# Performance work log

Measured on AMD Instinct MI355X. Metric: run time of the kernel, lower is better.

Reference implementation:

```python
import jax, jax.numpy as jnp
import numpy as np

N, D, E = 16384, 2048, 64   # tokens, d_model, num_experts
K = 9                        # self.k = min(k+1, num_experts) with k=8
EPS = 0.01
SIGMA = 1.0 / E              # Normal(0, 1/num_experts) stddev


def setup_inputs() -> dict:
    key = jax.random.key(0)
    ks = jax.random.split(key, 6)
    x = jax.random.normal(ks[0], (N, D), jnp.float32)
    Wr = jax.random.normal(ks[1], (D, E), jnp.float32) * 0.02
    br = jnp.zeros((E,), jnp.float32)
    Wn = jax.random.normal(ks[2], (D, E), jnp.float32) * 0.02
    bn = jnp.zeros((E,), jnp.float32)
    noise_eps = jax.random.normal(ks[3], (N, E), jnp.float32)
    # torch: (-empty.exponential_()).log() -> log of Exp(1) samples
    gumbel_noise = jnp.log(jax.random.exponential(ks[4], (N, E), jnp.float32))
    return {"x": x, "Wr": Wr, "br": br, "Wn": Wn, "bn": bn,
            "noise_eps": noise_eps, "gumbel_noise": gumbel_noise}


def reference(x, Wr, br, Wn, bn, noise_eps, gumbel_noise):
    raw_logits = x @ Wr + br                              # [N, E]
    noise_stddev = jax.nn.softplus(x @ Wn + bn) + EPS     # [N, E]
    noisy_logits = raw_logits + noise_eps * noise_stddev  # [N, E]

    top_vals, top_idx = jax.lax.top_k(noisy_logits, K)    # [N, K] sorted desc
    # scatter ones at top-k indices (indices unique per row)
    hard_mask = jax.nn.one_hot(top_idx, E, dtype=noisy_logits.dtype).sum(axis=1)  # [N, E]

    # gumbel-softmax straight-through relaxation
    mask_soft = jax.nn.softmax(noisy_logits + gumbel_noise, axis=-1)
    expert_mask = hard_mask - jax.lax.stop_gradient(mask_soft) + mask_soft

    route_prob = jax.nn.softmax(noisy_logits, axis=-1)    # [N, E]
    importance = jax.nn.softmax(raw_logits, axis=-1).sum(axis=0)  # [E]

    # load: P(raw + noise > threshold), Normal(0, 1/E) CDF per original
    threshold = top_vals[:, K - 1]                        # [N]
    z = (threshold[:, None] - raw_logits) / noise_stddev  # [N, E]
    cdf = 0.5 * (1.0 + jax.scipy.special.erf(z / (SIGMA * jnp.sqrt(jnp.float32(2.0)))))
    load = (1.0 - cdf).sum(axis=0)                        # [E]

    return (expert_mask, route_prob, importance, load)
```

## Files before the change

kernel.cpp:

```cpp
#include <hip/hip_runtime.h>
#include <hip/hip_bf16.h>
#include <math.h>

#define N_TOK 16384
#define DIM   2048
#define NE    64
#define TOPK  9

#define ROWS     32
#define DC       64
#define NCHUNK   (DIM / DC)
#define NTHREADS 256

typedef short  short8  __attribute__((ext_vector_type(8)));
typedef float  float4_ __attribute__((ext_vector_type(4)));
typedef unsigned short ushort_t;

__device__ __forceinline__ void async16(const void* g, void* l) {
    __builtin_amdgcn_global_load_lds(
        (const __attribute__((address_space(1))) void*)g,
        (__attribute__((address_space(3))) void*)l, 16, 0, 0);
}

__device__ __forceinline__ unsigned pk2(float a, float b) {
    float2 f; f.x = a; f.y = b;
    __hip_bfloat162 h = __float22bfloat162_rn(f);
    unsigned u;
    __builtin_memcpy(&u, &h, 4);
    return u;
}

__device__ __forceinline__ void cvt8(const float4_ va, const float4_ vb,
                                     short8* h, short8* l) {
    union { short8 s; unsigned u[4]; } H, L;
    const float f[8] = {va[0], va[1], va[2], va[3], vb[0], vb[1], vb[2], vb[3]};
#pragma unroll
    for (int i = 0; i < 4; ++i) {
        const float a = f[2 * i], b = f[2 * i + 1];
        const unsigned p = pk2(a, b);
        H.u[i] = p;
        const float ha = __uint_as_float(p << 16);
        const float hb = __uint_as_float(p & 0xffff0000u);
        L.u[i] = pk2(a - ha, b - hb);
    }
    *h = H.s; *l = L.s;
}

__device__ __forceinline__ float wave_max64(float v) {
#pragma unroll
    for (int off = 32; off > 0; off >>= 1)
        v = fmaxf(v, __shfl_xor(v, off, 64));
    return v;
}
__device__ __forceinline__ float wave_sum64(float v) {
#pragma unroll
    for (int off = 32; off > 0; off >>= 1)
        v += __shfl_xor(v, off, 64);
    return v;
}

__global__ __launch_bounds__(256)
void prep_w(const float* __restrict__ Wr, const float* __restrict__ Wn,
            ushort_t* __restrict__ wsW)
{
    const int gid = blockIdx.x * 256 + threadIdx.x;
    const int l   = gid & 63;
    const int ct  = (gid >> 6) & 7;
    const int kcg = gid >> 9;
    const int n   = ct * 16 + (l & 15);
    const int k0  = kcg * 32 + (l >> 4) * 8;
    const float* src = (n < NE) ? (Wr + n) : (Wn + (n - NE));
    union { short8 s; ushort_t us[8]; } H, L;
#pragma unroll
    for (int j = 0; j < 8; ++j) {
        const float v = src[(size_t)(k0 + j) * NE];
        const unsigned uv = __float_as_uint(v);
        const unsigned hb = (uv + 0x7fffu + ((uv >> 16) & 1u)) & 0xffff0000u;
        const float lo = v - __uint_as_float(hb);
        const unsigned ul = __float_as_uint(lo);
        H.us[j] = (ushort_t)(hb >> 16);
        L.us[j] = (ushort_t)((ul + 0x7fffu + ((ul >> 16) & 1u)) >> 16);
    }
    const size_t s0 = (size_t)(kcg * 8 + ct) * 2;
    *(short8*)(wsW + s0 * 512 + l * 8)         = H.s;
    *(short8*)(wsW + (s0 + 1) * 512 + l * 8)   = L.s;
}

__global__ __launch_bounds__(NTHREADS, 3)
void moe_main(const float* __restrict__ x,
              const float* __restrict__ br,
              const float* __restrict__ bn,
              const float* __restrict__ noise_eps,
              const float* __restrict__ gumbel,
              const ushort_t* __restrict__ wsW,
              float* __restrict__ out)
{
    __shared__ __align__(16) float smem[4352];

    const int t    = threadIdx.x;
    const int lane = t & 63;
    const int w    = t >> 6;
    const int c4   = lane & 15;
    const int q    = lane >> 4;
    const int row0 = blockIdx.x * ROWS;

    const float* gxp[2];
    int lxo[2];
#pragma unroll
    for (int ii = 0; ii < 2; ++ii) {
        const int i  = 2 * w + ii;
        const int r  = 4 * i + q;
        const int gk = c4 ^ (r & 15);
        gxp[ii] = x + (size_t)(row0 + r) * DIM + gk * 4;
        lxo[ii] = i * 256;
    }

    int aoff[2][2];
#pragma unroll
    for (int kc = 0; kc < 2; ++kc) {
        const int g0 = kc * 8 + q * 2;
        aoff[kc][0] = c4 * 64 + ((g0 ^ c4) * 4);
        aoff[kc][1] = c4 * 64 + (((g0 + 1) ^ c4) * 4);
    }

    float4_ acc[2][2];
#pragma unroll
    for (int rt = 0; rt < 2; ++rt)
#pragma unroll
        for (int cc = 0; cc < 2; ++cc)
            acc[rt][cc] = (float4_)(0.f);

    const char* wsB = (const char*)wsW;

#pragma unroll
    for (int ii = 0; ii < 2; ++ii) { async16(gxp[ii], &smem[lxo[ii]]); gxp[ii] += DC; }

    for (int ch = 0; ch < NCHUNK; ++ch) {
        __syncthreads();
        const int b = ch & 1;
        short8 bh[2][2], bl[2][2];
#pragma unroll
        for (int kc = 0; kc < 2; ++kc)
#pragma unroll
            for (int cc = 0; cc < 2; ++cc) {
                const size_t off = (size_t)(((ch * 2 + kc) * 8) + 2 * w + cc) * 2048 + lane * 16;
                bh[kc][cc] = *(const short8*)(wsB + off);
                bl[kc][cc] = *(const short8*)(wsB + off + 1024);
            }
        if (ch + 1 < NCHUNK) {
#pragma unroll
            for (int ii = 0; ii < 2; ++ii) {
                async16(gxp[ii], &smem[(b ^ 1) * 2048 + lxo[ii]]);
                gxp[ii] += DC;
            }
        }
        const float* xb = &smem[b * 2048];
#pragma unroll
        for (int kc = 0; kc < 2; ++kc)
#pragma unroll
            for (int rt = 0; rt < 2; ++rt) {
                const float4_ va = *(const float4_*)(xb + rt * 1024 + aoff[kc][0]);
                const float4_ vb = *(const float4_*)(xb + rt * 1024 + aoff[kc][1]);
                short8 ah, al;
                cvt8(va, vb, &ah, &al);
#pragma unroll
                for (int cc = 0; cc < 2; ++cc) {
                    acc[rt][cc] = __builtin_amdgcn_mfma_f32_16x16x32_bf16(ah, bh[kc][cc], acc[rt][cc], 0, 0, 0);
                    acc[rt][cc] = __builtin_amdgcn_mfma_f32_16x16x32_bf16(al, bh[kc][cc], acc[rt][cc], 0, 0, 0);
                    acc[rt][cc] = __builtin_amdgcn_mfma_f32_16x16x32_bf16(ah, bl[kc][cc], acc[rt][cc], 0, 0, 0);
                }
            }
    }

    __syncthreads();
    float* rawS = &smem[0];
    float* noiS = &smem[2080];
#pragma unroll
    for (int rt = 0; rt < 2; ++rt)
#pragma unroll
        for (int cc = 0; cc < 2; ++cc) {
            const int colg = (2 * w + cc) * 16 + c4;
            float* basep = (colg < NE) ? rawS : noiS;
            const int col = colg & 63;
#pragma unroll
            for (int v = 0; v < 4; ++v) {
                const int row = rt * 16 + q * 4 + v;
                basep[row * 65 + col] = acc[rt][cc][v];
            }
        }
    __syncthreads();

    const float br_l = br[lane];
    const float bn_l = bn[lane];
    float imp_acc = 0.f, load_acc = 0.f;
    float* out_em   = out;
    float* out_rp   = out + (size_t)N_TOK * NE;
    float* out_imp  = out + (size_t)2 * N_TOK * NE;
    float* out_load = out_imp + NE;

#pragma unroll 1
    for (int r = 0; r < 8; ++r) {
        const int lrow = w * 8 + r;
        const int row  = row0 + lrow;
        const float raw = rawS[lrow * 65 + lane] + br_l;
        const float nl  = noiS[lrow * 65 + lane] + bn_l;
        const float sd = fmaxf(nl, 0.f) + log1pf(expf(-fabsf(nl))) + 0.01f;
        const float epsv = noise_eps[(size_t)row * NE + lane];
        const float gum  = gumbel  [(size_t)row * NE + lane];
        const float noisy = fmaf(epsv, sd, raw);

        float cur = noisy;
        float thr = 0.f, m0 = 0.f;
#pragma unroll 1
        for (int k = 0; k < TOPK; ++k) {
            const float m = wave_max64(cur);
            if (k == 0) m0 = m;
            thr = m;
            const unsigned long long bm = __ballot(cur == m);
            const int first = __ffsll(bm) - 1;
            if (lane == first) cur = -INFINITY;
        }
        const float hard = (noisy >= thr) ? 1.f : 0.f;

        const float g  = noisy + gum;
        const float eg = expf(g - wave_max64(g));
        const float ms = eg / wave_sum64(eg);
        const float em = (hard - ms) + ms;

        const float en = expf(noisy - m0);
        const float rp = en / wave_sum64(en);

        const float er = expf(raw - wave_max64(raw));
        imp_acc += er / wave_sum64(er);

        const float z = (thr - raw) / sd;
        load_acc += 0.5f * erfcf(z * 45.254833995939045f);

        out_em[(size_t)row * NE + lane] = em;
        out_rp[(size_t)row * NE + lane] = rp;
    }

    __syncthreads();
    smem[w * 64 + lane]       = imp_acc;
    smem[256 + w * 64 + lane] = load_acc;
    __syncthreads();
    if (w == 0) {
        const float s1 = smem[lane] + smem[64 + lane] + smem[128 + lane] + smem[192 + lane];
        const float s2 = smem[256 + lane] + smem[320 + lane] + smem[384 + lane] + smem[448 + lane];
        atomicAdd(&out_imp[lane], s1);
        atomicAdd(&out_load[lane], s2);
    }
}

extern "C" void kernel_launch(void* const* d_in, const int* in_sizes, int n_in,
                              void* d_out, int out_size, void* d_ws, size_t ws_size,
                              hipStream_t stream)
{
    const float* x         = (const float*)d_in[0];
    const float* Wr        = (const float*)d_in[1];
    const float* br        = (const float*)d_in[2];
    const float* Wn        = (const float*)d_in[3];
    const float* bn        = (const float*)d_in[4];
    const float* noise_eps = (const float*)d_in[5];
    const float* gumbel    = (const float*)d_in[6];
    float* out = (float*)d_out;
    ushort_t* wsW = (ushort_t*)d_ws;

    (void)hipMemsetAsync((char*)d_out + (size_t)2 * N_TOK * NE * sizeof(float), 0,
                         2 * NE * sizeof(float), stream);
    prep_w<<<128, 256, 0, stream>>>(Wr, Wn, wsW);
    moe_main<<<N_TOK / ROWS, NTHREADS, 0, stream>>>(
        x, br, bn, noise_eps, gumbel, wsW, out);
}
```

Baseline: 268.5 us.

## Deepen x LDS pipeline to four buffers and prefetch weight fragments ahead

```diff
diff --git a/kernel.cpp b/kernel.cpp
--- a/kernel.cpp
+++ b/kernel.cpp
@@ -11,6 +11,7 @@
 #define DC       64
 #define NCHUNK   (DIM / DC)
 #define NTHREADS 256
+#define NBUF     4
 
 typedef short  short8  __attribute__((ext_vector_type(8)));
 typedef float  float4_ __attribute__((ext_vector_type(4)));
@@ -86,7 +87,43 @@
     *(short8*)(wsW + (s0 + 1) * 512 + l * 8)   = L.s;
 }
 
-__global__ __launch_bounds__(NTHREADS, 3)
+struct BFrag { short8 h[2][2]; short8 l[2][2]; };
+
+__device__ __forceinline__ void load_b(const char* __restrict__ wsB,
+                                       int ch, int w, int lane, BFrag& b) {
+#pragma unroll
+    for (int kc = 0; kc < 2; ++kc)
+#pragma unroll
+        for (int cc = 0; cc < 2; ++cc) {
+            const size_t off = (size_t)(((ch * 2 + kc) * 8) + 2 * w + cc) * 2048
+                             + (size_t)lane * 16;
+            b.h[kc][cc] = *(const short8*)(wsB + off);
+            b.l[kc][cc] = *(const short8*)(wsB + off + 1024);
+        }
+}
+
+__device__ __forceinline__ void mfma_chunk(const float* __restrict__ xb,
+                                           const int (&aoff)[2][2],
+                                           const BFrag& b,
+                                           float4_ (&acc)[2][2]) {
+#pragma unroll
+    for (int kc = 0; kc < 2; ++kc)
+#pragma unroll
+        for (int rt = 0; rt < 2; ++rt) {
+            const float4_ va = *(const float4_*)(xb + rt * 1024 + aoff[kc][0]);
+            const float4_ vb = *(const float4_*)(xb + rt * 1024 + aoff[kc][1]);
+            short8 ah, al;
+            cvt8(va, vb, &ah, &al);
+#pragma unroll
+            for (int cc = 0; cc < 2; ++cc) {
+                acc[rt][cc] = __builtin_amdgcn_mfma_f32_16x16x32_bf16(ah, b.h[kc][cc], acc[rt][cc], 0, 0, 0);
+                acc[rt][cc] = __builtin_amdgcn_mfma_f32_16x16x32_bf16(al, b.h[kc][cc], acc[rt][cc], 0, 0, 0);
+                acc[rt][cc] = __builtin_amdgcn_mfma_f32_16x16x32_bf16(ah, b.l[kc][cc], acc[rt][cc], 0, 0, 0);
+            }
+        }
+}
+
+__global__ __launch_bounds__(NTHREADS, 2)
 void moe_main(const float* __restrict__ x,
               const float* __restrict__ br,
               const float* __restrict__ bn,
@@ -95,7 +132,7 @@
               const ushort_t* __restrict__ wsW,
               float* __restrict__ out)
 {
-    __shared__ __align__(16) float smem[4352];
+    __shared__ __align__(16) float smem[NBUF * 2048];
 
     const int t    = threadIdx.x;
     const int lane = t & 63;
@@ -104,14 +141,14 @@
     const int q    = lane >> 4;
     const int row0 = blockIdx.x * ROWS;
 
-    const float* gxp[2];
+    const float* gxb[2];
     int lxo[2];
 #pragma unroll
     for (int ii = 0; ii < 2; ++ii) {
         const int i  = 2 * w + ii;
         const int r  = 4 * i + q;
         const int gk = c4 ^ (r & 15);
-        gxp[ii] = x + (size_t)(row0 + r) * DIM + gk * 4;
+        gxb[ii] = x + (size_t)(row0 + r) * DIM + gk * 4;
         lxo[ii] = i * 256;
     }
 
@@ -133,43 +170,41 @@
     const char* wsB = (const char*)wsW;
 
 #pragma unroll
-    for (int ii = 0; ii < 2; ++ii) { async16(gxp[ii], &smem[lxo[ii]]); gxp[ii] += DC; }
-
-    for (int ch = 0; ch < NCHUNK; ++ch) {
-        __syncthreads();
-        const int b = ch & 1;
-        short8 bh[2][2], bl[2][2];
-#pragma unroll
-        for (int kc = 0; kc < 2; ++kc)
-#pragma unroll
-            for (int cc = 0; cc < 2; ++cc) {
-                const size_t off = (size_t)(((ch * 2 + kc) * 8) + 2 * w + cc) * 2048 + lane * 16;
-                bh[kc][cc] = *(const short8*)(wsB + off);
-                bl[kc][cc] = *(const short8*)(wsB + off + 1024);
-            }
-        if (ch + 1 < NCHUNK) {
-#pragma unroll
-            for (int ii = 0; ii < 2; ++ii) {
-                async16(gxp[ii], &smem[(b ^ 1) * 2048 + lxo[ii]]);
-                gxp[ii] += DC;
-            }
-        }
-        const float* xb = &smem[b * 2048];
-#pragma unroll
-        for (int kc = 0; kc < 2; ++kc)
-#pragma unroll
-            for (int rt = 0; rt < 2; ++rt) {
-                const float4_ va = *(const float4_*)(xb + rt * 1024 + aoff[kc][0]);
-                const float4_ vb = *(const float4_*)(xb + rt * 1024 + aoff[kc][1]);
-                short8 ah, al;
-                cvt8(va, vb, &ah, &al);
-#pragma unroll
-                for (int cc = 0; cc < 2; ++cc) {
-                    acc[rt][cc] = __builtin_amdgcn_mfma_f32_16x16x32_bf16(ah, bh[kc][cc], acc[rt][cc], 0, 0, 0);
-                    acc[rt][cc] = __builtin_amdgcn_mfma_f32_16x16x32_bf16(al, bh[kc][cc], acc[rt][cc], 0, 0, 0);
-                    acc[rt][cc] = __builtin_amdgcn_mfma_f32_16x16x32_bf16(ah, bl[kc][cc], acc[rt][cc], 0, 0, 0);
-                }
-            }
+    for (int p = 0; p < NBUF - 1; ++p)
+#pragma unroll
+        for (int ii = 0; ii < 2; ++ii)
+            async16(gxb[ii] + p * DC, &smem[p * 2048 + lxo[ii]]);
+
+    BFrag bA, bB;
+    load_b(wsB, 0, w, lane, bA);
+
+#pragma unroll 1
+    for (int ch = 0; ch < NCHUNK; ch += 2) {
+        asm volatile("s_waitcnt vmcnt(12)" ::: "memory");
+        __builtin_amdgcn_s_barrier();
+        asm volatile("" ::: "memory");
+        load_b(wsB, (ch + 1 < NCHUNK) ? ch + 1 : NCHUNK - 1, w, lane, bB);
+        if (ch + NBUF - 1 < NCHUNK) {
+#pragma unroll
+            for (int ii = 0; ii < 2; ++ii)
+                async16(gxb[ii] + (ch + NBUF - 1) * DC,
+                        &smem[((ch + NBUF - 1) & (NBUF - 1)) * 2048 + lxo[ii]]);
+        }
+        __builtin_amdgcn_sched_barrier(0);
+        mfma_chunk(&smem[(ch & (NBUF - 1)) * 2048], aoff, bA, acc);
+
+        asm volatile("s_waitcnt vmcnt(12)" ::: "memory");
+        __builtin_amdgcn_s_barrier();
+        asm volatile("" ::: "memory");
+        load_b(wsB, (ch + 2 < NCHUNK) ? ch + 2 : NCHUNK - 1, w, lane, bA);
+        if (ch + NBUF < NCHUNK) {
+#pragma unroll
+            for (int ii = 0; ii < 2; ++ii)
+                async16(gxb[ii] + (ch + NBUF) * DC,
+                        &smem[((ch + NBUF) & (NBUF - 1)) * 2048 + lxo[ii]]);
+        }
+        __builtin_amdgcn_sched_barrier(0);
+        mfma_chunk(&smem[((ch + 1) & (NBUF - 1)) * 2048], aoff, bB, acc);
     }
 
     __syncthreads();
```

Result: faster. 257.0 us (-4.3%).
